# Kernel tuning notes

Measured on AMD Instinct MI355X. Metric: run time of the kernel, lower is better.

## Reference

```python
import jax, jax.numpy as jnp
from jax import lax
import numpy as np

N = 65536
D = 512
NUM_STEPS = 10
TIME_INTERVAL = 1.0


def setup_inputs() -> dict:
    key = jax.random.key(0)
    ks = jax.random.split(key, 8)
    s1 = 1.0 / np.sqrt(D + 1)
    s2 = 1.0 / np.sqrt(D)
    sg = 1.0 / np.sqrt(2 * D)
    return {
        "current_node_features": jax.random.normal(ks[0], (N, D), jnp.float32),
        "previous_hidden_state": jax.random.normal(ks[1], (N, D), jnp.float32),
        # torch nn.Linear layout: weight [out, in], bias [out]
        "W1": jax.random.uniform(ks[2], (D, D + 1), jnp.float32, -s1, s1),
        "b1": jax.random.uniform(ks[3], (D,), jnp.float32, -s1, s1),
        "W2": jax.random.uniform(ks[4], (D, D), jnp.float32, -s2, s2),
        "b2": jax.random.uniform(ks[5], (D,), jnp.float32, -s2, s2),
        "Wg": jax.random.uniform(ks[6], (D, 2 * D), jnp.float32, -sg, sg),
        "bg": jax.random.uniform(ks[7], (D,), jnp.float32, -sg, sg),
    }


def reference(current_node_features, previous_hidden_state, W1, b1, W2, b2, Wg, bg):
    x = current_node_features
    dt = jnp.asarray(TIME_INTERVAL / NUM_STEPS, x.dtype)
    n = x.shape[0]

    def euler_step(h, t):
        # concat time feature: [N, D+1]
        time_col = jnp.full((n, 1), t, h.dtype)
        z = jnp.concatenate([h, time_col], axis=-1)
        deriv = jnp.tanh(jnp.tanh(z @ W1.T + b1) @ W2.T + b2)
        return h + dt * deriv, None

    ts = jnp.arange(NUM_STEPS, dtype=x.dtype) * dt  # t_i = start + i*dt
    evolved, _ = lax.scan(euler_step, previous_hidden_state, ts)

    combined = jnp.concatenate([x, evolved], axis=-1)  # [N, 2D]
    gate = jax.nn.sigmoid(combined @ Wg.T + bg)
    updated = gate * evolved + (1.0 - gate) * x
    return updated, updated
```

## Files before the change

### kernel.cpp

```cpp
#include <hip/hip_runtime.h>

#define N_ROWS 65536
#define DIM    512
#define NSTEP  10

typedef float  f32x16 __attribute__((ext_vector_type(16)));
typedef float  f32x4  __attribute__((ext_vector_type(4)));
typedef short  s16x8  __attribute__((ext_vector_type(8)));
typedef __bf16 bf16x8 __attribute__((ext_vector_type(8)));
typedef unsigned int u32x2 __attribute__((ext_vector_type(2)));
typedef unsigned int u32x4 __attribute__((ext_vector_type(4)));

__device__ __forceinline__ unsigned f2bf(float f) {
  unsigned u = __float_as_uint(f);
  return (u + 0x7fffu + ((u >> 16) & 1u)) >> 16;
}
__device__ __forceinline__ unsigned pack2bf_rn(float a, float b) {
  unsigned ua = __float_as_uint(a) + 0x8000u;
  unsigned ub = __float_as_uint(b) + 0x8000u;
  return __builtin_amdgcn_perm(ub, ua, 0x07060302u);
}
#define LOG2E_X2 2.885390081777927f
#define LOG2E    1.442695040888963f
__device__ __forceinline__ float ftanh(float x) {
  float t = __builtin_amdgcn_exp2f(x * LOG2E_X2);
  float r = __builtin_amdgcn_rcpf(1.0f + t);
  return __builtin_fmaf(-2.0f, r, 1.0f);
}
__device__ __forceinline__ float fsigm(float x) {
  float t = __builtin_amdgcn_exp2f(-x * LOG2E);
  return __builtin_amdgcn_rcpf(1.0f + t);
}
__device__ __forceinline__ void mfma(f32x16& c, s16x8 a, s16x8 b) {
  c = __builtin_amdgcn_mfma_f32_32x32x16_bf16(
        __builtin_bit_cast(bf16x8, a), __builtin_bit_cast(bf16x8, b), c, 0, 0, 0);
}

__global__ void pack_frags_kernel(const float* __restrict__ src, int row_stride,
                                  int col_off, unsigned short* __restrict__ dst) {
  const int idx = blockIdx.x * 256 + threadIdx.x;
  const int l    = idx & 63;
  const int frag = idx >> 6;
  const int ks   = frag >> 4;
  const int otg  = frag & 15;
  const int o = otg * 32 + (l & 31);
  const int k = ks * 16 + (l >> 5) * 8;
  const float* p = src + (size_t)o * row_stride + col_off + k;
  s16x8 v;
#pragma unroll
  for (int i = 0; i < 8; ++i) v[i] = (short)f2bf(p[i]);
  *reinterpret_cast<s16x8*>(dst + (size_t)idx * 8) = v;
}

__global__ void c1_kernel(const float* __restrict__ W1, const float* __restrict__ b1,
                          float* __restrict__ c1) {
  const int o = threadIdx.x;
  const float wt = W1[(size_t)o * 513 + 512];
  const float bb = b1[o];
  for (int s = 0; s < NSTEP; ++s)
    c1[s * DIM + o] = bb + ((float)s * 0.1f) * wt;
}

__global__ __launch_bounds__(512, 2)
void ode_fused(const float* __restrict__ x, const float* __restrict__ h0,
               const float* __restrict__ b2, const float* __restrict__ bg,
               const unsigned short* __restrict__ w1f, const unsigned short* __restrict__ w2f,
               const unsigned short* __restrict__ wgaf, const unsigned short* __restrict__ wgbf,
               const float* __restrict__ c1, float* __restrict__ out)
{
  __shared__ char ldsT[64 * 1024];

  const int tid = threadIdx.x;
  const int w   = tid >> 6;
  const int l   = tid & 63;
  const int lm  = l & 31;
  const int h5  = l >> 5;
  const int m0  = blockIdx.x << 6;
  const int ow  = w << 6;
  const int rot = blockIdx.x & 31;

  {
    const int r  = tid >> 3;
    const int c0 = (tid & 7) << 2;
    const float* src = h0 + (size_t)(m0 + r) * DIM;
    char* trow = ldsT + r * 1024;
    const unsigned sw = (r & 7) << 4;
#pragma unroll
    for (int j = 0; j < 16; ++j) {
      const int c = c0 + j * 32;
      f32x4 v = *reinterpret_cast<const f32x4*>(src + c);
      u32x2 pk;
      pk[0] = pack2bf_rn(v[0], v[1]);
      pk[1] = pack2bf_rn(v[2], v[3]);
      *reinterpret_cast<u32x2*>(trow + (((unsigned)(c << 1)) ^ sw)) = pk;
    }
  }

  f32x16 hst[2][2];
#pragma unroll
  for (int ot = 0; ot < 2; ++ot)
#pragma unroll
    for (int mt = 0; mt < 2; ++mt) {
      const float* hr = h0 + (size_t)(m0 + (mt << 5) + lm) * DIM;
#pragma unroll
      for (int g = 0; g < 4; ++g) {
        const int oc = ow + (ot << 5) + (g << 3) + (h5 << 2);
        f32x4 v = *reinterpret_cast<const f32x4*>(hr + oc);
#pragma unroll
        for (int j = 0; j < 4; ++j) hst[ot][mt][(g << 2) + j] = v[j];
      }
    }

  const unsigned bm0 = (unsigned)lm << 10;
  const unsigned bm1 = (unsigned)(lm + 32) << 10;
  const unsigned sxm = (lm & 7) << 4;
  const unsigned kh  = (unsigned)h5 << 4;

  f32x16 acc[2][2];

  auto mm_lds = [&](const unsigned short* __restrict__ AF, const char* buf) {
    const s16x8* A = reinterpret_cast<const s16x8*>(AF);
#pragma unroll 4
    for (int ks = 0; ks < 32; ++ks) {
      const int kk = (ks + rot) & 31;
      const int fb = ((kk << 4) + (w << 1)) << 6;
      s16x8 a0 = A[fb + l];
      s16x8 a1 = A[fb + 64 + l];
      const unsigned ko = (((unsigned)kk << 5) + kh) ^ sxm;
      s16x8 b0 = *reinterpret_cast<const s16x8*>(buf + (bm0 + ko));
      s16x8 b1 = *reinterpret_cast<const s16x8*>(buf + (bm1 + ko));
      mfma(acc[0][0], a0, b0);
      mfma(acc[0][1], a0, b1);
      mfma(acc[1][0], a1, b0);
      mfma(acc[1][1], a1, b1);
    }
  };

  auto acc_init = [&](const float* __restrict__ vec) {
#pragma unroll
    for (int ot = 0; ot < 2; ++ot)
#pragma unroll
      for (int g = 0; g < 4; ++g) {
        const int oc = ow + (ot << 5) + (g << 3) + (h5 << 2);
        f32x4 v = *reinterpret_cast<const f32x4*>(vec + oc);
#pragma unroll
        for (int mt = 0; mt < 2; ++mt)
#pragma unroll
          for (int j = 0; j < 4; ++j) acc[ot][mt][(g << 2) + j] = v[j];
      }
  };

  auto tile_write = [&](const f32x16 src[2][2], char* buf) {
#pragma unroll
    for (int mt = 0; mt < 2; ++mt) {
      const unsigned m = (unsigned)((mt << 5) + lm);
      char* trow = buf + (m << 10);
      const unsigned sw = (m & 7) << 4;
#pragma unroll
      for (int ot = 0; ot < 2; ++ot)
#pragma unroll
        for (int g = 0; g < 4; ++g) {
          const unsigned oc = (unsigned)(ow + (ot << 5) + (g << 3) + (h5 << 2));
          u32x2 pk;
          pk[0] = pack2bf_rn(src[ot][mt][(g << 2) + 0], src[ot][mt][(g << 2) + 1]);
          pk[1] = pack2bf_rn(src[ot][mt][(g << 2) + 2], src[ot][mt][(g << 2) + 3]);
          *reinterpret_cast<u32x2*>(trow + ((oc << 1) ^ sw)) = pk;
        }
    }
  };

  __syncthreads();

  for (int s = 0; s < NSTEP; ++s) {
    acc_init(c1 + s * DIM);
    mm_lds(w1f, ldsT);
#pragma unroll
    for (int ot = 0; ot < 2; ++ot)
#pragma unroll
      for (int mt = 0; mt < 2; ++mt)
#pragma unroll
        for (int i = 0; i < 16; ++i) acc[ot][mt][i] = ftanh(acc[ot][mt][i]);
    __syncthreads();
    tile_write(acc, ldsT);
    __syncthreads();
    acc_init(b2);
    mm_lds(w2f, ldsT);
#pragma unroll
    for (int ot = 0; ot < 2; ++ot)
#pragma unroll
      for (int mt = 0; mt < 2; ++mt)
#pragma unroll
        for (int i = 0; i < 16; ++i) {
          float t = __builtin_amdgcn_exp2f(acc[ot][mt][i] * LOG2E_X2);
          float r = __builtin_amdgcn_rcpf(1.0f + t);
          hst[ot][mt][i] = __builtin_fmaf(-0.2f, r, hst[ot][mt][i] + 0.1f);
        }
    __syncthreads();
    tile_write(hst, ldsT);
    __syncthreads();
  }

  acc_init(bg);
  mm_lds(wgbf, ldsT);
  {
    const s16x8* A = reinterpret_cast<const s16x8*>(wgaf);
    const float* xr0 = x + (size_t)(m0 + lm) * DIM;
    const float* xr1 = x + (size_t)(m0 + 32 + lm) * DIM;
#pragma unroll 2
    for (int ks = 0; ks < 32; ++ks) {
      const int kk = (ks + rot) & 31;
      const int fb = ((kk << 4) + (w << 1)) << 6;
      s16x8 a0 = A[fb + l];
      s16x8 a1 = A[fb + 64 + l];
      const int kc = (kk << 4) + (h5 << 3);
      f32x4 u0 = *reinterpret_cast<const f32x4*>(xr0 + kc);
      f32x4 u1 = *reinterpret_cast<const f32x4*>(xr0 + kc + 4);
      u32x4 pb;
      pb[0] = pack2bf_rn(u0[0], u0[1]); pb[1] = pack2bf_rn(u0[2], u0[3]);
      pb[2] = pack2bf_rn(u1[0], u1[1]); pb[3] = pack2bf_rn(u1[2], u1[3]);
      s16x8 b0 = __builtin_bit_cast(s16x8, pb);
      f32x4 w0 = *reinterpret_cast<const f32x4*>(xr1 + kc);
      f32x4 w1 = *reinterpret_cast<const f32x4*>(xr1 + kc + 4);
      u32x4 qb;
      qb[0] = pack2bf_rn(w0[0], w0[1]); qb[1] = pack2bf_rn(w0[2], w0[3]);
      qb[2] = pack2bf_rn(w1[0], w1[1]); qb[3] = pack2bf_rn(w1[2], w1[3]);
      s16x8 b1 = __builtin_bit_cast(s16x8, qb);
      mfma(acc[0][0], a0, b0);
      mfma(acc[0][1], a0, b1);
      mfma(acc[1][0], a1, b0);
      mfma(acc[1][1], a1, b1);
    }
  }

  float* out1 = out + (size_t)N_ROWS * DIM;
#pragma unroll
  for (int mt = 0; mt < 2; ++mt) {
    const int m = m0 + (mt << 5) + lm;
    const float* xr = x + (size_t)m * DIM;
    float* o0p = out  + (size_t)m * DIM;
    float* o1p = out1 + (size_t)m * DIM;
#pragma unroll
    for (int ot = 0; ot < 2; ++ot)
#pragma unroll
      for (int g = 0; g < 4; ++g) {
        const int oc = ow + (ot << 5) + (g << 3) + (h5 << 2);
        f32x4 xv = *reinterpret_cast<const f32x4*>(xr + oc);
        f32x4 r;
#pragma unroll
        for (int j = 0; j < 4; ++j) {
          const float gt = fsigm(acc[ot][mt][(g << 2) + j]);
          const float ev = hst[ot][mt][(g << 2) + j];
          r[j] = gt * ev + (1.0f - gt) * xv[j];
        }
        *reinterpret_cast<f32x4*>(o0p + oc) = r;
        *reinterpret_cast<f32x4*>(o1p + oc) = r;
      }
  }
}

extern "C" void kernel_launch(void* const* d_in, const int* in_sizes, int n_in,
                              void* d_out, int out_size, void* d_ws, size_t ws_size,
                              hipStream_t stream) {
  const float* x  = (const float*)d_in[0];
  const float* h0 = (const float*)d_in[1];
  const float* W1 = (const float*)d_in[2];
  const float* b1 = (const float*)d_in[3];
  const float* W2 = (const float*)d_in[4];
  const float* b2 = (const float*)d_in[5];
  const float* Wg = (const float*)d_in[6];
  const float* bg = (const float*)d_in[7];

  char* ws = (char*)d_ws;
  const size_t FRAG_BYTES = (size_t)512 * 512 * 2;
  unsigned short* w1f  = (unsigned short*)(ws + 0 * FRAG_BYTES);
  unsigned short* w2f  = (unsigned short*)(ws + 1 * FRAG_BYTES);
  unsigned short* wgaf = (unsigned short*)(ws + 2 * FRAG_BYTES);
  unsigned short* wgbf = (unsigned short*)(ws + 3 * FRAG_BYTES);
  float*          c1   = (float*)(ws + 4 * FRAG_BYTES);

  pack_frags_kernel<<<128, 256, 0, stream>>>(W1, 513, 0,   w1f);
  pack_frags_kernel<<<128, 256, 0, stream>>>(W2, 512, 0,   w2f);
  pack_frags_kernel<<<128, 256, 0, stream>>>(Wg, 1024, 0,  wgaf);
  pack_frags_kernel<<<128, 256, 0, stream>>>(Wg, 1024, 512, wgbf);
  c1_kernel<<<1, 512, 0, stream>>>(W1, b1, c1);

  ode_fused<<<N_ROWS / 64, 512, 0, stream>>>(x, h0, b2, bg, w1f, w2f, wgaf, wgbf,
                                             c1, (float*)d_out);
}
```

Before: 960.0 us.

## Split output columns across 16 waves per block instead of 8

Doubles the block to 1024 threads so each wave computes a 32-column output slice rather than 64, halving per-wave accumulator and hidden-state registers and the weight-fragment loads per wave. The aim is more waves in flight per CU to hide LDS and global latency during the chained matmuls. In exchange, each B fragment read from LDS is shared by fewer MFMAs, so LDS traffic per flop doubles. Larger blocks also make each __syncthreads barrier more costly, and the launch-bounds hint for two blocks per CU is dropped.

```diff
diff --git a/kernel.cpp b/kernel.cpp
--- a/kernel.cpp
+++ b/kernel.cpp
@@ -61,7 +61,7 @@
     c1[s * DIM + o] = bb + ((float)s * 0.1f) * wt;
 }
 
-__global__ __launch_bounds__(512, 2)
+__global__ __launch_bounds__(1024)
 void ode_fused(const float* __restrict__ x, const float* __restrict__ h0,
                const float* __restrict__ b2, const float* __restrict__ bg,
                const unsigned short* __restrict__ w1f, const unsigned short* __restrict__ w2f,
@@ -76,18 +76,18 @@
   const int lm  = l & 31;
   const int h5  = l >> 5;
   const int m0  = blockIdx.x << 6;
-  const int ow  = w << 6;
+  const int ow  = w << 5;
   const int rot = blockIdx.x & 31;
 
   {
-    const int r  = tid >> 3;
-    const int c0 = (tid & 7) << 2;
+    const int r  = tid >> 4;
+    const int c0 = (tid & 15) << 2;
     const float* src = h0 + (size_t)(m0 + r) * DIM;
     char* trow = ldsT + r * 1024;
     const unsigned sw = (r & 7) << 4;
 #pragma unroll
-    for (int j = 0; j < 16; ++j) {
-      const int c = c0 + j * 32;
+    for (int j = 0; j < 8; ++j) {
+      const int c = c0 + (j << 6);
       f32x4 v = *reinterpret_cast<const f32x4*>(src + c);
       u32x2 pk;
       pk[0] = pack2bf_rn(v[0], v[1]);
@@ -96,76 +96,67 @@
     }
   }
 
-  f32x16 hst[2][2];
-#pragma unroll
-  for (int ot = 0; ot < 2; ++ot)
-#pragma unroll
-    for (int mt = 0; mt < 2; ++mt) {
-      const float* hr = h0 + (size_t)(m0 + (mt << 5) + lm) * DIM;
-#pragma unroll
-      for (int g = 0; g < 4; ++g) {
-        const int oc = ow + (ot << 5) + (g << 3) + (h5 << 2);
-        f32x4 v = *reinterpret_cast<const f32x4*>(hr + oc);
-#pragma unroll
-        for (int j = 0; j < 4; ++j) hst[ot][mt][(g << 2) + j] = v[j];
-      }
-    }
+  f32x16 hst[2];
+#pragma unroll
+  for (int mt = 0; mt < 2; ++mt) {
+    const float* hr = h0 + (size_t)(m0 + (mt << 5) + lm) * DIM;
+#pragma unroll
+    for (int g = 0; g < 4; ++g) {
+      const int oc = ow + (g << 3) + (h5 << 2);
+      f32x4 v = *reinterpret_cast<const f32x4*>(hr + oc);
+#pragma unroll
+      for (int j = 0; j < 4; ++j) hst[mt][(g << 2) + j] = v[j];
+    }
+  }
 
   const unsigned bm0 = (unsigned)lm << 10;
   const unsigned bm1 = (unsigned)(lm + 32) << 10;
   const unsigned sxm = (lm & 7) << 4;
   const unsigned kh  = (unsigned)h5 << 4;
 
-  f32x16 acc[2][2];
+  f32x16 acc[2];
 
   auto mm_lds = [&](const unsigned short* __restrict__ AF, const char* buf) {
     const s16x8* A = reinterpret_cast<const s16x8*>(AF);
 #pragma unroll 4
     for (int ks = 0; ks < 32; ++ks) {
       const int kk = (ks + rot) & 31;
-      const int fb = ((kk << 4) + (w << 1)) << 6;
-      s16x8 a0 = A[fb + l];
-      s16x8 a1 = A[fb + 64 + l];
+      s16x8 a = A[(((kk << 4) + w) << 6) + l];
       const unsigned ko = (((unsigned)kk << 5) + kh) ^ sxm;
       s16x8 b0 = *reinterpret_cast<const s16x8*>(buf + (bm0 + ko));
       s16x8 b1 = *reinterpret_cast<const s16x8*>(buf + (bm1 + ko));
-      mfma(acc[0][0], a0, b0);
-      mfma(acc[0][1], a0, b1);
-      mfma(acc[1][0], a1, b0);
-      mfma(acc[1][1], a1, b1);
+      mfma(acc[0], a, b0);
+      mfma(acc[1], a, b1);
     }
   };
 
   auto acc_init = [&](const float* __restrict__ vec) {
 #pragma unroll
-    for (int ot = 0; ot < 2; ++ot)
-#pragma unroll
-      for (int g = 0; g < 4; ++g) {
-        const int oc = ow + (ot << 5) + (g << 3) + (h5 << 2);
-        f32x4 v = *reinterpret_cast<const f32x4*>(vec + oc);
-#pragma unroll
-        for (int mt = 0; mt < 2; ++mt)
-#pragma unroll
-          for (int j = 0; j < 4; ++j) acc[ot][mt][(g << 2) + j] = v[j];
-      }
+    for (int g = 0; g < 4; ++g) {
+      const int oc = ow + (g << 3) + (h5 << 2);
+      f32x4 v = *reinterpret_cast<const f32x4*>(vec + oc);
+#pragma unroll
+      for (int j = 0; j < 4; ++j) {
+        acc[0][(g << 2) + j] = v[j];
+        acc[1][(g << 2) + j] = v[j];
+      }
+    }
   };
 
-  auto tile_write = [&](const f32x16 src[2][2], char* buf) {
+  auto tile_write = [&](const f32x16 src[2], char* buf) {
 #pragma unroll
     for (int mt = 0; mt < 2; ++mt) {
       const unsigned m = (unsigned)((mt << 5) + lm);
       char* trow = buf + (m << 10);
       const unsigned sw = (m & 7) << 4;
 #pragma unroll
-      for (int ot = 0; ot < 2; ++ot)
-#pragma unroll
-        for (int g = 0; g < 4; ++g) {
-          const unsigned oc = (unsigned)(ow + (ot << 5) + (g << 3) + (h5 << 2));
-          u32x2 pk;
-          pk[0] = pack2bf_rn(src[ot][mt][(g << 2) + 0], src[ot][mt][(g << 2) + 1]);
-          pk[1] = pack2bf_rn(src[ot][mt][(g << 2) + 2], src[ot][mt][(g << 2) + 3]);
-          *reinterpret_cast<u32x2*>(trow + ((oc << 1) ^ sw)) = pk;
-        }
+      for (int g = 0; g < 4; ++g) {
+        const unsigned oc = (unsigned)(ow + (g << 3) + (h5 << 2));
+        u32x2 pk;
+        pk[0] = pack2bf_rn(src[mt][(g << 2) + 0], src[mt][(g << 2) + 1]);
+        pk[1] = pack2bf_rn(src[mt][(g << 2) + 2], src[mt][(g << 2) + 3]);
+        *reinterpret_cast<u32x2*>(trow + ((oc << 1) ^ sw)) = pk;
+      }
     }
   };
 
@@ -175,26 +166,22 @@
     acc_init(c1 + s * DIM);
     mm_lds(w1f, ldsT);
 #pragma unroll
-    for (int ot = 0; ot < 2; ++ot)
-#pragma unroll
-      for (int mt = 0; mt < 2; ++mt)
-#pragma unroll
-        for (int i = 0; i < 16; ++i) acc[ot][mt][i] = ftanh(acc[ot][mt][i]);
+    for (int mt = 0; mt < 2; ++mt)
+#pragma unroll
+      for (int i = 0; i < 16; ++i) acc[mt][i] = ftanh(acc[mt][i]);
     __syncthreads();
     tile_write(acc, ldsT);
     __syncthreads();
     acc_init(b2);
     mm_lds(w2f, ldsT);
 #pragma unroll
-    for (int ot = 0; ot < 2; ++ot)
-#pragma unroll
-      for (int mt = 0; mt < 2; ++mt)
-#pragma unroll
-        for (int i = 0; i < 16; ++i) {
-          float t = __builtin_amdgcn_exp2f(acc[ot][mt][i] * LOG2E_X2);
-          float r = __builtin_amdgcn_rcpf(1.0f + t);
-          hst[ot][mt][i] = __builtin_fmaf(-0.2f, r, hst[ot][mt][i] + 0.1f);
-        }
+    for (int mt = 0; mt < 2; ++mt)
+#pragma unroll
+      for (int i = 0; i < 16; ++i) {
+        float t = __builtin_amdgcn_exp2f(acc[mt][i] * LOG2E_X2);
+        float r = __builtin_amdgcn_rcpf(1.0f + t);
+        hst[mt][i] = __builtin_fmaf(-0.2f, r, hst[mt][i] + 0.1f);
+      }
     __syncthreads();
     tile_write(hst, ldsT);
     __syncthreads();
@@ -209,9 +196,7 @@
 #pragma unroll 2
     for (int ks = 0; ks < 32; ++ks) {
       const int kk = (ks + rot) & 31;
-      const int fb = ((kk << 4) + (w << 1)) << 6;
-      s16x8 a0 = A[fb + l];
-      s16x8 a1 = A[fb + 64 + l];
+      s16x8 a = A[(((kk << 4) + w) << 6) + l];
       const int kc = (kk << 4) + (h5 << 3);
       f32x4 u0 = *reinterpret_cast<const f32x4*>(xr0 + kc);
       f32x4 u1 = *reinterpret_cast<const f32x4*>(xr0 + kc + 4);
@@ -225,10 +210,8 @@
       qb[0] = pack2bf_rn(w0[0], w0[1]); qb[1] = pack2bf_rn(w0[2], w0[3]);
       qb[2] = pack2bf_rn(w1[0], w1[1]); qb[3] = pack2bf_rn(w1[2], w1[3]);
       s16x8 b1 = __builtin_bit_cast(s16x8, qb);
-      mfma(acc[0][0], a0, b0);
-      mfma(acc[0][1], a0, b1);
-      mfma(acc[1][0], a1, b0);
-      mfma(acc[1][1], a1, b1);
+      mfma(acc[0], a, b0);
+      mfma(acc[1], a, b1);
     }
   }
 
@@ -240,21 +223,19 @@
     float* o0p = out  + (size_t)m * DIM;
     float* o1p = out1 + (size_t)m * DIM;
 #pragma unroll
-    for (int ot = 0; ot < 2; ++ot)
-#pragma unroll
-      for (int g = 0; g < 4; ++g) {
-        const int oc = ow + (ot << 5) + (g << 3) + (h5 << 2);
-        f32x4 xv = *reinterpret_cast<const f32x4*>(xr + oc);
-        f32x4 r;
-#pragma unroll
-        for (int j = 0; j < 4; ++j) {
-          const float gt = fsigm(acc[ot][mt][(g << 2) + j]);
-          const float ev = hst[ot][mt][(g << 2) + j];
-          r[j] = gt * ev + (1.0f - gt) * xv[j];
-        }
-        *reinterpret_cast<f32x4*>(o0p + oc) = r;
-        *reinterpret_cast<f32x4*>(o1p + oc) = r;
-      }
+    for (int g = 0; g < 4; ++g) {
+      const int oc = ow + (g << 3) + (h5 << 2);
+      f32x4 xv = *reinterpret_cast<const f32x4*>(xr + oc);
+      f32x4 r;
+#pragma unroll
+      for (int j = 0; j < 4; ++j) {
+        const float gt = fsigm(acc[mt][(g << 2) + j]);
+        const float ev = hst[mt][(g << 2) + j];
+        r[j] = gt * ev + (1.0f - gt) * xv[j];
+      }
+      *reinterpret_cast<f32x4*>(o0p + oc) = r;
+      *reinterpret_cast<f32x4*>(o1p + oc) = r;
+    }
   }
 }
 
@@ -284,6 +265,6 @@
   pack_frags_kernel<<<128, 256, 0, stream>>>(Wg, 1024, 512, wgbf);
   c1_kernel<<<1, 512, 0, stream>>>(W1, b1, c1);
 
-  ode_fused<<<N_ROWS / 64, 512, 0, stream>>>(x, h0, b2, bg, w1f, w2f, wgaf, wgbf,
-                                             c1, (float*)d_out);
-}
+  ode_fused<<<N_ROWS / 64, 1024, 0, stream>>>(x, h0, b2, bg, w1f, w2f, wgaf, wgbf,
+                                              c1, (float*)d_out);
+}
```

New measurement: 1.048 ms. 9.2% more time.
